# Optimization experiments

Measured on AMD Instinct MI355X. Metric: run time of the kernel, lower is better.

The kernel has to match this reference:

```python
import jax, jax.numpy as jnp
import numpy as np
import math

B, N, D = 8, 4096, 768
H, M, L = 12, 64, 4
HD = D // H  # 64
TEMP = 1.0
EPS = 1e-5


def layer_norm(x, g, b):
    m = jnp.mean(x, axis=-1, keepdims=True)
    v = jnp.mean((x - m) ** 2, axis=-1, keepdims=True)
    return (x - m) * jax.lax.rsqrt(v + EPS) * g + b


def setup_inputs() -> dict:
    key = jax.random.key(0)
    ks = jax.random.split(key, 24)
    s = 0.02
    inp = {
        "latent_tokens": jax.random.normal(ks[0], (B, N, D), jnp.float32),
        "selector": jax.random.normal(ks[1], (M, D), jnp.float32) * s,
        "qc": jax.random.normal(ks[2], (L, M, D), jnp.float32) * s,
        "qw": jax.random.normal(ks[3], (L, H, D, HD), jnp.float32) * s,
        "qb": jnp.zeros((L, H, HD), jnp.float32),
        "kw": jax.random.normal(ks[4], (L, H, D, HD), jnp.float32) * s,
        "kb": jnp.zeros((L, H, HD), jnp.float32),
        "vw": jax.random.normal(ks[5], (L, H, D, HD), jnp.float32) * s,
        "vb": jnp.zeros((L, H, HD), jnp.float32),
        "hw": jax.random.normal(ks[6], (L, H, HD, HD), jnp.float32) * s,
        "hb": jnp.zeros((L, H, HD), jnp.float32),
        "ow": jax.random.normal(ks[7], (L, D, D), jnp.float32) * s,
        "ob": jnp.zeros((L, D), jnp.float32),
        "w1": jax.random.normal(ks[8], (L, D, 4 * D), jnp.float32) * s,
        "b1": jnp.zeros((L, 4 * D), jnp.float32),
        "w2": jax.random.normal(ks[9], (L, 4 * D, D), jnp.float32) * s,
        "b2": jnp.zeros((L, D), jnp.float32),
        "g1": jnp.ones((L, D), jnp.float32),
        "beta1": jnp.zeros((L, D), jnp.float32),
        "g2": jnp.ones((L, D), jnp.float32),
        "beta2": jnp.zeros((L, D), jnp.float32),
    }
    return inp


def reference(latent_tokens, selector, qc, qw, qb, kw, kb, vw, vb, hw, hb,
              ow, ob, w1, b1, w2, b2, g1, beta1, g2, beta2):
    scale = 1.0 / math.sqrt(HD)
    # soft-selection pooling of encoder tokens into M pos queries
    logits = jnp.einsum('bnd,md->bmn', latent_tokens, selector)
    weights = jax.nn.softmax(logits / TEMP, axis=-1)
    x = jnp.einsum('bmn,bnd->bmd', weights, latent_tokens)  # [B,M,D]
    for l in range(L):
        queries = qc[l][None] + x                                    # [B,M,D]
        q = jnp.einsum('bmd,hde->bhme', queries, qw[l]) + qb[l][None, :, None, :]
        k = jnp.einsum('bnd,hde->bhne', latent_tokens, kw[l]) + kb[l][None, :, None, :]
        v = jnp.einsum('bnd,hde->bhne', latent_tokens, vw[l]) + vb[l][None, :, None, :]
        attn = jax.nn.softmax(jnp.einsum('bhme,bhne->bhmn', q, k) * scale, axis=-1)
        o = jnp.einsum('bhmn,bhne->bhme', attn, v)                   # [B,H,M,HD]
        o = jnp.einsum('bhme,hef->bhmf', o, hw[l]) + hb[l][None, :, None, :]
        o = o.transpose(0, 2, 1, 3).reshape(o.shape[0], M, D)        # concat heads
        o = o @ ow[l] + ob[l]
        x1 = layer_norm(o + queries, g1[l], beta1[l])
        mlp = jax.nn.gelu(x1 @ w1[l] + b1[l], approximate=False) @ w2[l] + b2[l]
        x = layer_norm(x1 + mlp, g2[l], beta2[l])
    return x
```

## Files before the change

### kernel.cpp

```cpp
#include <hip/hip_runtime.h>
#include <hip/hip_bf16.h>


using bf16 = __hip_bfloat16;
typedef __attribute__((ext_vector_type(8))) __bf16 bf16x8;
typedef __attribute__((ext_vector_type(4))) float f32x4;
typedef unsigned int u32;
typedef __attribute__((ext_vector_type(4))) u32 u32x4;

#define DEVINL __device__ __forceinline__

DEVINL float bf2f(bf16 v) { return __bfloat162float(v); }
DEVINL bf16 f2bf(float v) { return __float2bfloat16(v); }
DEVINL u32 f2bfu(float f) { bf16 h = __float2bfloat16(f); return *(unsigned short*)&h; }
DEVINL float gelu_f(float x) { return 0.5f * x * (1.0f + erff(x * 0.70710678118654752f)); }

DEVINL void async16(const bf16* g, bf16* l) {
  __builtin_amdgcn_global_load_lds(
      (const __attribute__((address_space(1))) u32*)g,
      (__attribute__((address_space(3))) u32*)l, 16, 0, 0);
}

DEVINL u32 xcd_swizzle(u32 id, u32 nwg) {
  u32 q = nwg >> 3, r = nwg & 7;
  u32 xcd = id & 7, pos = id >> 3;
  return xcd * q + (xcd < r ? xcd : r) + pos;
}

__global__ __launch_bounds__(256) void cvt_f2b(const float* in, bf16* out, long n) {
  const long i = ((long)blockIdx.x * 256 + threadIdx.x) * 8;
  if (i >= n) return;
  float4 a = *(const float4*)(in + i);
  float4 b = *(const float4*)(in + i + 4);
  u32 w[4];
  w[0] = f2bfu(a.x) | (f2bfu(a.y) << 16);
  w[1] = f2bfu(a.z) | (f2bfu(a.w) << 16);
  w[2] = f2bfu(b.x) | (f2bfu(b.y) << 16);
  w[3] = f2bfu(b.z) | (f2bfu(b.w) << 16);
  *(u32x4*)(out + i) = *(u32x4*)w;
}

struct GemmKVP {
  const bf16* A;
  const bf16* Bk;
  const bf16* Bv;
  bf16* Ck;
  bf16* Cv;
  const float* biask;
  const float* biasv;
};

__global__ __launch_bounds__(256, 2) void gemm_kv(GemmKVP p) {
  __shared__ __align__(16) bf16 SH[40960];
  bf16* As = SH;
  bf16* Ks = SH + 16384;
  bf16* Vs = SH + 28672;
  const int tid = threadIdx.x;
  const int wave = tid >> 6, lane = tid & 63;

  u32 id = blockIdx.x + 6u * blockIdx.y;
  id = xcd_swizzle(id, 1536);
  const int bn = id % 6;
  const int bm = id / 6;

  const bf16* Ag = p.A + (long)bm * 128 * 768;
  const bf16* Kg = p.Bk + (long)bn * 128 * 768;
  const bf16* Vg = p.Bv + (long)bn * 128 * 768;

  const int cq = (((tid & 3) ^ ((tid >> 3) & 3))) * 8;
  const long ro = (long)(tid >> 2) * 768 + cq;
  const long r1 = ro + (long)64 * 768;
  const bf16* ga0 = Ag + ro; const bf16* ga1 = Ag + r1;
  const bf16* gk0 = Kg + ro; const bf16* gk1 = Kg + r1;
  const bf16* gv0 = Vg + ro; const bf16* gv1 = Vg + r1;

  const int m_in = lane & 15, q = lane >> 4;
  const int wm = (wave & 1) * 64, wn = (wave >> 1) * 64;
  const int sw3 = (q ^ ((m_in >> 1) & 3)) << 3;
  f32x4 acck[4][4] = {};
  f32x4 accv[4][4] = {};
  const int nk = 24;

  auto stageA = [&](int s, int ko) {
    async16(ga0 + ko, As + s * 4096 + tid * 8);
    async16(ga1 + ko, As + s * 4096 + 2048 + tid * 8);
  };
  auto stageKV = [&](int s, int ko) {
    async16(gk0 + ko, Ks + s * 4096 + tid * 8);
    async16(gk1 + ko, Ks + s * 4096 + 2048 + tid * 8);
    async16(gv0 + ko, Vs + s * 4096 + tid * 8);
    async16(gv1 + ko, Vs + s * 4096 + 2048 + tid * 8);
  };
  stageA(0, 0); stageA(1, 32); stageKV(0, 0); stageA(2, 64); stageKV(1, 32);

  for (int k = 0; k < nk; ++k) {
    if (k < nk - 2)       asm volatile("s_waitcnt vmcnt(6)" ::: "memory");
    else if (k == nk - 2) asm volatile("s_waitcnt vmcnt(4)" ::: "memory");
    else                  asm volatile("s_waitcnt vmcnt(0)" ::: "memory");
    __builtin_amdgcn_s_barrier();
    if (k + 3 < nk) stageA((k + 3) & 3, (k + 3) * 32);
    if (k + 2 < nk) stageKV((k + 2) % 3, (k + 2) * 32);
    const bf16* Ac = As + (k & 3) * 4096;
    const bf16* Kc = Ks + (k % 3) * 4096;
    const bf16* Vc = Vs + (k % 3) * 4096;
    bf16x8 af[4], bfr[4];
#pragma unroll
    for (int i = 0; i < 4; i++)
      af[i] = *(const bf16x8*)(Ac + (wm + i * 16 + m_in) * 32 + sw3);
#pragma unroll
    for (int j = 0; j < 4; j++)
      bfr[j] = *(const bf16x8*)(Kc + (wn + j * 16 + m_in) * 32 + sw3);
#pragma unroll
    for (int i = 0; i < 4; i++)
#pragma unroll
      for (int j = 0; j < 4; j++)
        acck[i][j] = __builtin_amdgcn_mfma_f32_16x16x32_bf16(af[i], bfr[j], acck[i][j], 0, 0, 0);
#pragma unroll
    for (int j = 0; j < 4; j++)
      bfr[j] = *(const bf16x8*)(Vc + (wn + j * 16 + m_in) * 32 + sw3);
#pragma unroll
    for (int i = 0; i < 4; i++)
#pragma unroll
      for (int j = 0; j < 4; j++)
        accv[i][j] = __builtin_amdgcn_mfma_f32_16x16x32_bf16(af[i], bfr[j], accv[i][j], 0, 0, 0);
  }

  const long row0 = (long)bm * 128 + wm + q * 4;
  const long col0 = (long)bn * 128 + wn + m_in;
  const int bb = (bm * 128) >> 12;
  const int nn0 = (bm * 128) & 4095;
#pragma unroll
  for (int i = 0; i < 4; i++)
#pragma unroll
    for (int j = 0; j < 4; j++) {
      long r = row0 + i * 16;
      long c = col0 + j * 16;
      float bk_ = p.biask[c];
#pragma unroll
      for (int t = 0; t < 4; t++)
        p.Ck[(r + t) * 768 + c] = f2bf(acck[i][j][t] + bk_);
    }
  __syncthreads();
  bf16* VT = SH;
#pragma unroll
  for (int i = 0; i < 4; i++) {
    const int nb = wm + q * 4 + i * 16;
    const int sl = nb >> 3;
    const int of = nb & 7;
#pragma unroll
    for (int j = 0; j < 4; j++) {
      const int e = wn + j * 16 + m_in;
      const float bv_ = p.biasv[bn * 128 + e];
      u32 w0 = f2bfu(accv[i][j][0] + bv_) | (f2bfu(accv[i][j][1] + bv_) << 16);
      u32 w1 = f2bfu(accv[i][j][2] + bv_) | (f2bfu(accv[i][j][3] + bv_) << 16);
      uint2 pk; pk.x = w0; pk.y = w1;
      *(uint2*)(VT + e * 128 + ((sl ^ (e & 15)) << 3) + of) = pk;
    }
  }
  __syncthreads();
  bf16* CvB = p.Cv + (long)bb * 3145728;
#pragma unroll
  for (int k2 = 0; k2 < 8; k2++) {
    int g = tid + k2 * 256;
    int e = g >> 4, sc = g & 15;
    u32x4 vv = *(const u32x4*)(VT + e * 128 + ((sc ^ (e & 15)) << 3));
    *(u32x4*)(CvB + (long)(bn * 128 + e) * 4096 + nn0 + sc * 8) = vv;
  }
}

struct GemmSmP {
  const bf16* A; const bf16* B; void* C; const float* bias; const float* res;
  long sA1, sA2, sB1, sB2, sC1, sC2, sBias2;
  int nb2, lda, ldb, ldc, K;
  int bias_mode;
  int out_mode;
  float scale;
};

__global__ __launch_bounds__(256, 4) void gemm_sm(GemmSmP p) {
  __shared__ __align__(16) bf16 As[3][64 * 32];
  __shared__ __align__(16) bf16 Bs[3][64 * 32];
  const int tid = threadIdx.x;
  const int wave = tid >> 6, lane = tid & 63;

  const u32 gx = gridDim.x, gy = gridDim.y;
  u32 id = blockIdx.x + gx * (blockIdx.y + gy * blockIdx.z);
  id = xcd_swizzle(id, gx * gy * gridDim.z);
  const int bn = id % gx;
  const u32 t2 = id / gx;
  const int bm = t2 % gy;
  const int bz = t2 / gy;

  const int z1 = bz / p.nb2, z2 = bz - z1 * p.nb2;
  const bf16* Ag = p.A + p.sA1 * z1 + p.sA2 * z2 + (long)bm * 64 * p.lda;
  const bf16* Bg = p.B + p.sB1 * z1 + p.sB2 * z2 + (long)bn * 64 * p.ldb;

  const int cq = (((tid & 3) ^ ((tid >> 3) & 3))) * 8;
  const bf16* gpa = Ag + ((long)(tid >> 2) * p.lda + cq);
  const bf16* gpb = Bg + ((long)(tid >> 2) * p.ldb + cq);

  const int m_in = lane & 15, q = lane >> 4;
  const int wm = (wave & 1) * 32, wn = (wave >> 1) * 32;
  const int sw3 = (q ^ ((m_in >> 1) & 3)) << 3;
  f32x4 acc[2][2] = {};
  const int nk = p.K >> 5;

  async16(gpa, &As[0][0] + tid * 8);
  async16(gpb, &Bs[0][0] + tid * 8);
  if (nk > 1) {
    async16(gpa + 32, &As[1][0] + tid * 8);
    async16(gpb + 32, &Bs[1][0] + tid * 8);
  }

  int slot = 0;
  for (int k = 0; k < nk; ++k) {
    if (k + 1 < nk) asm volatile("s_waitcnt vmcnt(2)" ::: "memory");
    else            asm volatile("s_waitcnt vmcnt(0)" ::: "memory");
    __builtin_amdgcn_s_barrier();
    if (k + 2 < nk) {
      int ns = slot + 2; if (ns >= 3) ns -= 3;
      const int ko = (k + 2) * 32;
      async16(gpa + ko, &As[ns][0] + tid * 8);
      async16(gpb + ko, &Bs[ns][0] + tid * 8);
    }
    const bf16* Ac = &As[slot][0];
    const bf16* Bc = &Bs[slot][0];
    bf16x8 a0 = *(const bf16x8*)(Ac + (wm + m_in) * 32 + sw3);
    bf16x8 a1 = *(const bf16x8*)(Ac + (wm + 16 + m_in) * 32 + sw3);
    bf16x8 b0 = *(const bf16x8*)(Bc + (wn + m_in) * 32 + sw3);
    bf16x8 b1 = *(const bf16x8*)(Bc + (wn + 16 + m_in) * 32 + sw3);
    acc[0][0] = __builtin_amdgcn_mfma_f32_16x16x32_bf16(a0, b0, acc[0][0], 0, 0, 0);
    acc[0][1] = __builtin_amdgcn_mfma_f32_16x16x32_bf16(a0, b1, acc[0][1], 0, 0, 0);
    acc[1][0] = __builtin_amdgcn_mfma_f32_16x16x32_bf16(a1, b0, acc[1][0], 0, 0, 0);
    acc[1][1] = __builtin_amdgcn_mfma_f32_16x16x32_bf16(a1, b1, acc[1][1], 0, 0, 0);
    slot = (slot + 1 == 3) ? 0 : slot + 1;
  }

  const long row0 = (long)bm * 64 + wm + q * 4;
  const long col0 = (long)bn * 64 + wn + m_in;
  const float* bias = p.bias + p.sBias2 * z2;
#pragma unroll
  for (int i = 0; i < 2; i++)
#pragma unroll
    for (int j = 0; j < 2; j++) {
      long r = row0 + i * 16;
      long cc = col0 + j * 16;
      float badd = (p.bias_mode == 1) ? bias[cc] : 0.f;
#pragma unroll
      for (int t = 0; t < 4; t++) {
        float v = acc[i][j][t] * p.scale + badd;
        long idx = (r + t) * p.ldc + cc;
        if (p.out_mode == 0) {
          float* Cf = (float*)p.C + p.sC1 * z1 + p.sC2 * z2;
          if (p.res) v += p.res[idx];
          Cf[idx] = v;
        } else {
          bf16* Cb = (bf16*)p.C + p.sC1 * z1 + p.sC2 * z2;
          if (p.out_mode == 2) v = gelu_f(v);
          Cb[idx] = f2bf(v);
        }
      }
    }
}

struct AttnP {
  const bf16* Q;
  const bf16* K;
  const bf16* VT;
  float* Opart;
  float* ML;
};

__global__ __launch_bounds__(256, 3) void attn_part(AttnP p) {
  __shared__ __align__(16) bf16 SH[24576];
  bf16* Qs = SH;
  bf16* Ks = SH + 4096;
  bf16* Vs = SH + 12288;
  bf16* Ps = SH + 20480;
  const int tid = threadIdx.x;
  const int wave = tid >> 6, lane = tid & 63;
  const int z = blockIdx.x, c = blockIdx.y;
  const int b = z / 12, h = z - b * 12;
  const int n0 = c * 512;

  const int sl0 = tid, sl1 = tid + 256;
  const int r0 = sl0 >> 3, r1 = sl1 >> 3;
  const int q0 = (sl0 & 7) ^ (r0 & 7), q1 = (sl1 & 7) ^ (r1 & 7);

  const bf16* Qg = p.Q + ((long)b * 64) * 768 + h * 64;
  const bf16* Kg = p.K + ((long)b * 4096 + n0) * 768 + h * 64;
  const bf16* Vg = p.VT + (long)b * 3145728 + (long)(h * 64) * 4096 + n0;

  async16(Qg + (long)r0 * 768 + q0 * 8, Qs + sl0 * 8);
  async16(Qg + (long)r1 * 768 + q1 * 8, Qs + sl1 * 8);
  auto stageK = [&](int s) {
    bf16* d = Ks + (s & 1) * 4096;
    async16(Kg + (long)(s * 64 + r0) * 768 + q0 * 8, d + sl0 * 8);
    async16(Kg + (long)(s * 64 + r1) * 768 + q1 * 8, d + sl1 * 8);
  };
  auto stageV = [&](int s) {
    bf16* d = Vs + (s & 1) * 4096;
    async16(Vg + (long)r0 * 4096 + s * 64 + q0 * 8, d + sl0 * 8);
    async16(Vg + (long)r1 * 4096 + s * 64 + q1 * 8, d + sl1 * 8);
  };
  stageK(0); stageV(0); stageK(1); stageV(1);

  const int m_in = lane & 15, q = lane >> 4;
  const int wm = wave * 16;

  asm volatile("s_waitcnt vmcnt(8)" ::: "memory");
  __builtin_amdgcn_s_barrier();

  bf16x8 qa[2];
  {
    const int ra = wm + m_in;
#pragma unroll
    for (int kk = 0; kk < 2; kk++)
      qa[kk] = *(const bf16x8*)(Qs + ra * 64 + ((((kk * 4 + q) ^ (ra & 7))) << 3));
  }

  f32x4 accO[4] = {};
  float m_run[4] = {-1e30f, -1e30f, -1e30f, -1e30f};
  float l_run[4] = {0.f, 0.f, 0.f, 0.f};

  for (int s = 0; s < 8; ++s) {
    if (s < 7) asm volatile("s_waitcnt vmcnt(4)" ::: "memory");
    else       asm volatile("s_waitcnt vmcnt(0)" ::: "memory");
    __builtin_amdgcn_s_barrier();
    const bf16* Kc = Ks + (s & 1) * 4096;
    const bf16* Vc = Vs + (s & 1) * 4096;
    f32x4 accS[4] = {};
#pragma unroll
    for (int kk = 0; kk < 2; kk++) {
#pragma unroll
      for (int j = 0; j < 4; j++) {
        const int rj = j * 16 + m_in;
        bf16x8 kb = *(const bf16x8*)(Kc + rj * 64 + ((((kk * 4 + q) ^ (rj & 7))) << 3));
        accS[j] = __builtin_amdgcn_mfma_f32_16x16x32_bf16(qa[kk], kb, accS[j], 0, 0, 0);
      }
    }
    float pe[4][4], osc[4];
#pragma unroll
    for (int t = 0; t < 4; t++) {
      float mx = fmaxf(fmaxf(accS[0][t], accS[1][t]), fmaxf(accS[2][t], accS[3][t])) * 0.125f;
      mx = fmaxf(mx, __shfl_xor(mx, 1));
      mx = fmaxf(mx, __shfl_xor(mx, 2));
      mx = fmaxf(mx, __shfl_xor(mx, 4));
      mx = fmaxf(mx, __shfl_xor(mx, 8));
      const float mnew = fmaxf(m_run[t], mx);
      const float so = __expf(m_run[t] - mnew);
      float rs = 0.f;
#pragma unroll
      for (int j = 0; j < 4; j++) {
        float e = __expf(accS[j][t] * 0.125f - mnew);
        pe[j][t] = e; rs += e;
      }
      rs += __shfl_xor(rs, 1); rs += __shfl_xor(rs, 2);
      rs += __shfl_xor(rs, 4); rs += __shfl_xor(rs, 8);
      l_run[t] = l_run[t] * so + rs;
      m_run[t] = mnew;
      osc[t] = so;
    }
#pragma unroll
    for (int ef = 0; ef < 4; ef++)
#pragma unroll
      for (int t = 0; t < 4; t++) accO[ef][t] *= osc[t];
#pragma unroll
    for (int j = 0; j < 4; j++) {
      const int pc = m_in + 16 * j;
#pragma unroll
      for (int t = 0; t < 4; t++) {
        const int pm = wm + q * 4 + t;
        Ps[pm * 64 + (((pc >> 3) ^ (pm & 7)) << 3) + (pc & 7)] = f2bf(pe[j][t]);
      }
    }
    const int ra = wm + m_in;
#pragma unroll
    for (int kk = 0; kk < 2; kk++) {
      bf16x8 pa = *(const bf16x8*)(Ps + ra * 64 + ((((kk * 4 + q) ^ (ra & 7))) << 3));
#pragma unroll
      for (int ef = 0; ef < 4; ef++) {
        const int rv = ef * 16 + m_in;
        bf16x8 vb = *(const bf16x8*)(Vc + rv * 64 + ((((kk * 4 + q) ^ (rv & 7))) << 3));
        accO[ef] = __builtin_amdgcn_mfma_f32_16x16x32_bf16(pa, vb, accO[ef], 0, 0, 0);
      }
    }
    __builtin_amdgcn_s_barrier();
    if (s < 6) { stageK(s + 2); stageV(s + 2); }
  }

  float* Og = p.Opart + ((long)c * 96 + z) * 4096;
#pragma unroll
  for (int ef = 0; ef < 4; ef++)
#pragma unroll
    for (int t = 0; t < 4; t++)
      Og[(wm + q * 4 + t) * 64 + ef * 16 + m_in] = accO[ef][t];
  if (m_in == 0) {
    float* ml = p.ML + ((long)c * 96 + z) * 128;
#pragma unroll
    for (int t = 0; t < 4; t++) {
      ml[wm + q * 4 + t] = m_run[t];
      ml[64 + wm + q * 4 + t] = l_run[t];
    }
  }
}

struct AttnHMP {
  const float* Opart;
  const float* ML;
  const bf16* HWT;
  const float* hb;
  bf16* O2;
};

__global__ __launch_bounds__(256) void attn_hm(AttnHMP p) {
  __shared__ __align__(16) bf16 Os[4096];
  __shared__ __align__(16) bf16 Hs[4096];
  const int tid = threadIdx.x;
  const int z = blockIdx.x;
  const int b = z / 12, h = z - b * 12;

  const int sl0 = tid, sl1 = tid + 256;
  const int r0 = sl0 >> 3, r1 = sl1 >> 3;
  const int q0 = (sl0 & 7) ^ (r0 & 7), q1 = (sl1 & 7) ^ (r1 & 7);
  const bf16* Hg = p.HWT + h * 4096;
  async16(Hg + r0 * 64 + q0 * 8, Hs + sl0 * 8);
  async16(Hg + r1 * 64 + q1 * 8, Hs + sl1 * 8);

  const int m = tid >> 2, e0 = (tid & 3) * 16;
  float mv[8];
  float mx = -1e30f;
#pragma unroll
  for (int c = 0; c < 8; c++) {
    mv[c] = p.ML[((long)c * 96 + z) * 128 + m];
    mx = fmaxf(mx, mv[c]);
  }
  float l = 0.f;
  float o[16] = {};
#pragma unroll
  for (int c = 0; c < 8; c++) {
    const float w = __expf(mv[c] - mx);
    l += w * p.ML[((long)c * 96 + z) * 128 + 64 + m];
    const float* Og = p.Opart + (((long)c * 96 + z) * 64 + m) * 64 + e0;
#pragma unroll
    for (int e = 0; e < 16; e++) o[e] += w * Og[e];
  }
  const float inv = 1.f / l;
#pragma unroll
  for (int half = 0; half < 2; half++) {
    u32 wbuf[4];
#pragma unroll
    for (int j = 0; j < 4; j++)
      wbuf[j] = f2bfu(o[half * 8 + 2 * j] * inv) | (f2bfu(o[half * 8 + 2 * j + 1] * inv) << 16);
    const int sl = (e0 >> 3) + half;
    *(u32x4*)(Os + m * 64 + ((sl ^ (m & 7)) << 3)) = *(u32x4*)wbuf;
  }
  asm volatile("s_waitcnt vmcnt(0)" ::: "memory");
  __syncthreads();

  const int wave = tid >> 6, lane = tid & 63;
  const int m_in = lane & 15, q = lane >> 4;
  const int wm = wave * 16;
  f32x4 acc[4] = {};
#pragma unroll
  for (int kk = 0; kk < 2; kk++) {
    const int ra = wm + m_in;
    bf16x8 a = *(const bf16x8*)(Os + ra * 64 + ((((kk * 4 + q) ^ (ra & 7))) << 3));
#pragma unroll
    for (int j = 0; j < 4; j++) {
      const int rb = j * 16 + m_in;
      bf16x8 bv = *(const bf16x8*)(Hs + rb * 64 + ((((kk * 4 + q) ^ (rb & 7))) << 3));
      acc[j] = __builtin_amdgcn_mfma_f32_16x16x32_bf16(a, bv, acc[j], 0, 0, 0);
    }
  }
  bf16* O2r = p.O2 + ((long)b * 64) * 768 + h * 64;
#pragma unroll
  for (int j = 0; j < 4; j++) {
    const int e2 = j * 16 + m_in;
    const float badd = p.hb[h * 64 + e2];
#pragma unroll
    for (int t = 0; t < 4; t++)
      O2r[(wm + q * 4 + t) * 768 + e2] = f2bf(acc[j][t] + badd);
  }
}

struct TrP { const float* in; bf16* out; bf16* outR; int R, C; long sIn, sOut, sOutR; };

__global__ __launch_bounds__(256) void transpose_f2b(TrP p) {
  __shared__ __align__(16) bf16 tile[64][80];
  const int tid = threadIdx.x;
  const int ct = blockIdx.x, rt = blockIdx.y, z = blockIdx.z;
  const float* in = p.in + p.sIn * z + ((long)rt * 64) * p.C + (long)ct * 64;
  bf16* out = p.out + p.sOut * z + ((long)ct * 64) * p.R + (long)rt * 64;
  bf16* outR = p.outR ? p.outR + p.sOutR * z + ((long)rt * 64) * p.C + (long)ct * 64 : nullptr;
  const int r = tid >> 3, c8 = (tid & 7) * 8;
#pragma unroll
  for (int h = 0; h < 2; h++) {
    int rr = r + h * 32;
    float4 a = *(const float4*)(in + (long)rr * p.C + c8);
    float4 b = *(const float4*)(in + (long)rr * p.C + c8 + 4);
    u32 w[4];
    w[0] = f2bfu(a.x) | (f2bfu(a.y) << 16);
    w[1] = f2bfu(a.z) | (f2bfu(a.w) << 16);
    w[2] = f2bfu(b.x) | (f2bfu(b.y) << 16);
    w[3] = f2bfu(b.z) | (f2bfu(b.w) << 16);
    *(u32x4*)&tile[rr][c8] = *(u32x4*)w;
    if (outR) *(u32x4*)(outR + (long)rr * p.C + c8) = *(u32x4*)w;
  }
  __syncthreads();
  const int co = tid >> 3, r8 = (tid & 7) * 8;
#pragma unroll
  for (int h = 0; h < 2; h++) {
    int cc = co + h * 32;
    __align__(16) bf16 tmp[8];
#pragma unroll
    for (int j = 0; j < 8; j++) tmp[j] = tile[r8 + j][cc];
    *(u32x4*)(out + (long)cc * p.R + r8) = *(const u32x4*)tmp;
  }
}

__global__ __launch_bounds__(256) void softmax_rows(bf16* X) {
  const long row = blockIdx.x;
  u32* x = (u32*)(X + row * 4096);
  const int tid = threadIdx.x;
  const int lane = tid & 63, wave = tid >> 6;
  u32 d[8];
  *(u32x4*)&d[0] = ((const u32x4*)x)[tid * 2];
  *(u32x4*)&d[4] = ((const u32x4*)x)[tid * 2 + 1];
  float v[16];
#pragma unroll
  for (int j = 0; j < 8; j++) {
    v[2 * j] = __uint_as_float(d[j] << 16);
    v[2 * j + 1] = __uint_as_float(d[j] & 0xffff0000u);
  }
  float m = v[0];
#pragma unroll
  for (int i = 1; i < 16; i++) m = fmaxf(m, v[i]);
  for (int off = 32; off; off >>= 1) m = fmaxf(m, __shfl_xor(m, off));
  __shared__ float sm1[4], sm2[4];
  if (lane == 0) sm1[wave] = m;
  __syncthreads();
  m = fmaxf(fmaxf(sm1[0], sm1[1]), fmaxf(sm1[2], sm1[3]));
  float s = 0.f;
#pragma unroll
  for (int i = 0; i < 16; i++) { v[i] = __expf(v[i] - m); s += v[i]; }
  for (int off = 32; off; off >>= 1) s += __shfl_xor(s, off);
  if (lane == 0) sm2[wave] = s;
  __syncthreads();
  s = sm2[0] + sm2[1] + sm2[2] + sm2[3];
  const float inv = 1.f / s;
#pragma unroll
  for (int j = 0; j < 8; j++) {
    u32 lo = f2bfu(v[2 * j] * inv);
    u32 hi = f2bfu(v[2 * j + 1] * inv);
    d[j] = lo | (hi << 16);
  }
  ((u32x4*)x)[tid * 2] = *(u32x4*)&d[0];
  ((u32x4*)x)[tid * 2 + 1] = *(u32x4*)&d[4];
}

__global__ __launch_bounds__(256) void ln_rows(const float* in, const float* g, const float* b,
                                               float* outf, bf16* outb,
                                               const float* qc, float* qf, bf16* qb16) {
  const long row = blockIdx.x;
  const float* x = in + row * 768;
  const int tid = threadIdx.x;
  const int lane = tid & 63, wave = tid >> 6;
  float v0 = x[tid], v1 = x[tid + 256], v2 = x[tid + 512];
  float s = v0 + v1 + v2;
  float s2 = v0 * v0 + v1 * v1 + v2 * v2;
  for (int off = 32; off; off >>= 1) { s += __shfl_xor(s, off); s2 += __shfl_xor(s2, off); }
  __shared__ float sa[4], sb[4];
  if (lane == 0) { sa[wave] = s; sb[wave] = s2; }
  __syncthreads();
  s = sa[0] + sa[1] + sa[2] + sa[3];
  s2 = sb[0] + sb[1] + sb[2] + sb[3];
  const float mean = s * (1.f / 768.f);
  const float var = s2 * (1.f / 768.f) - mean * mean;
  const float rs = rsqrtf(var + 1e-5f);
  float o0 = (v0 - mean) * rs * g[tid] + b[tid];
  float o1 = (v1 - mean) * rs * g[tid + 256] + b[tid + 256];
  float o2 = (v2 - mean) * rs * g[tid + 512] + b[tid + 512];
  if (outf) { float* of = outf + row * 768; of[tid] = o0; of[tid + 256] = o1; of[tid + 512] = o2; }
  if (outb) { bf16* ob = outb + row * 768; ob[tid] = f2bf(o0); ob[tid + 256] = f2bf(o1); ob[tid + 512] = f2bf(o2); }
  if (qc) {
    const float* qr = qc + (row & 63) * 768;
    float u0 = o0 + qr[tid], u1 = o1 + qr[tid + 256], u2 = o2 + qr[tid + 512];
    float* pf = qf + row * 768;
    pf[tid] = u0; pf[tid + 256] = u1; pf[tid + 512] = u2;
    bf16* pb = qb16 + row * 768;
    pb[tid] = f2bf(u0); pb[tid + 256] = f2bf(u1); pb[tid + 512] = f2bf(u2);
  }
}

struct CombLnP {
  const float* in; int nch; const float* bias; const float* res;
  const float* g; const float* b;
  float* outf; bf16* outb;
  const float* qc; float* qf; bf16* qb16;
};

__global__ __launch_bounds__(256) void comb_ln(CombLnP p) {
  const long row = blockIdx.x;
  const long base = row * 768;
  const int tid = threadIdx.x;
  const int lane = tid & 63, wave = tid >> 6;
  float v0 = 0.f, v1 = 0.f, v2 = 0.f;
  for (int c = 0; c < p.nch; c++) {
    const float* x = p.in + (long)c * 393216 + base;
    v0 += x[tid]; v1 += x[tid + 256]; v2 += x[tid + 512];
  }
  v0 += p.bias[tid]; v1 += p.bias[tid + 256]; v2 += p.bias[tid + 512];
  if (p.res) {
    const float* r = p.res + base;
    v0 += r[tid]; v1 += r[tid + 256]; v2 += r[tid + 512];
  }
  float s = v0 + v1 + v2;
  float s2 = v0 * v0 + v1 * v1 + v2 * v2;
  for (int off = 32; off; off >>= 1) { s += __shfl_xor(s, off); s2 += __shfl_xor(s2, off); }
  __shared__ float sa[4], sb[4];
  if (lane == 0) { sa[wave] = s; sb[wave] = s2; }
  __syncthreads();
  s = sa[0] + sa[1] + sa[2] + sa[3];
  s2 = sb[0] + sb[1] + sb[2] + sb[3];
  const float mean = s * (1.f / 768.f);
  const float var = s2 * (1.f / 768.f) - mean * mean;
  const float rs = rsqrtf(var + 1e-5f);
  float o0 = (v0 - mean) * rs * p.g[tid] + p.b[tid];
  float o1 = (v1 - mean) * rs * p.g[tid + 256] + p.b[tid + 256];
  float o2 = (v2 - mean) * rs * p.g[tid + 512] + p.b[tid + 512];
  if (p.outf) { float* of = p.outf + base; of[tid] = o0; of[tid + 256] = o1; of[tid + 512] = o2; }
  if (p.outb) { bf16* ob = p.outb + base; ob[tid] = f2bf(o0); ob[tid + 256] = f2bf(o1); ob[tid + 512] = f2bf(o2); }
  if (p.qc) {
    const float* qr = p.qc + (row & 63) * 768;
    float u0 = o0 + qr[tid], u1 = o1 + qr[tid + 256], u2 = o2 + qr[tid + 512];
    float* pf = p.qf + base;
    pf[tid] = u0; pf[tid + 256] = u1; pf[tid + 512] = u2;
    bf16* pb = p.qb16 + base;
    pb[tid] = f2bf(u0); pb[tid + 256] = f2bf(u1); pb[tid + 512] = f2bf(u2);
  }
}

struct CombP { const float* in; int nch; const float* bias; const float* res;
               float* outf; bf16* outb; const float* qc; float* qf; bf16* qb16; };

__global__ __launch_bounds__(256) void combine(CombP p) {
  const long i = (long)blockIdx.x * 256 + threadIdx.x;
  float s = 0.f;
  for (int c = 0; c < p.nch; c++) s += p.in[(long)c * 393216 + i];
  if (p.bias) s += p.bias[i % 768];
  if (p.res) s += p.res[i];
  if (p.outf) p.outf[i] = s;
  if (p.outb) p.outb[i] = f2bf(s);
  if (p.qc) {
    float v = s + p.qc[i % 49152];
    p.qf[i] = v;
    p.qb16[i] = f2bf(v);
  }
}

extern "C" void kernel_launch(void* const* d_in, const int* in_sizes, int n_in,
                              void* d_out, int out_size, void* d_ws, size_t ws_size,
                              hipStream_t stream) {
  (void)in_sizes; (void)n_in; (void)out_size; (void)ws_size;
  const float* tokens   = (const float*)d_in[0];
  const float* selector = (const float*)d_in[1];
  const float* qc  = (const float*)d_in[2];
  const float* qw  = (const float*)d_in[3];
  const float* qb  = (const float*)d_in[4];
  const float* kw  = (const float*)d_in[5];
  const float* kb  = (const float*)d_in[6];
  const float* vw  = (const float*)d_in[7];
  const float* vb  = (const float*)d_in[8];
  const float* hw  = (const float*)d_in[9];
  const float* hb  = (const float*)d_in[10];
  const float* ow  = (const float*)d_in[11];
  const float* ob  = (const float*)d_in[12];
  const float* w1  = (const float*)d_in[13];
  const float* b1  = (const float*)d_in[14];
  const float* w2  = (const float*)d_in[15];
  const float* b2  = (const float*)d_in[16];
  const float* g1  = (const float*)d_in[17];
  const float* be1 = (const float*)d_in[18];
  const float* g2  = (const float*)d_in[19];
  const float* be2 = (const float*)d_in[20];
  float* out = (float*)d_out;

  char* ws = (char*)d_ws;
  size_t off = 0;
  auto alloc = [&](size_t bytes) { char* pp = ws + off; off += (bytes + 255) & ~(size_t)255; return pp; };
  bf16* TOKT  = (bf16*)alloc(50331648);
  bf16* TOKB  = (bf16*)alloc(50331648);
  bf16* KBUF  = (bf16*)alloc(50331648);
  bf16* VTB   = (bf16*)alloc(50331648);
  bf16* PLOG  = (bf16*)alloc(4194304);
  bf16* SELB  = (bf16*)alloc(98304);
  bf16* QWT   = (bf16*)alloc(4718592);
  bf16* KWT   = (bf16*)alloc(4718592);
  bf16* VWT   = (bf16*)alloc(4718592);
  bf16* HWT   = (bf16*)alloc(393216);
  bf16* OWT   = (bf16*)alloc(4718592);
  bf16* W1T   = (bf16*)alloc(18874368);
  bf16* W2T   = (bf16*)alloc(18874368);
  bf16* QBUF  = (bf16*)alloc(786432);
  bf16* O2BUF = (bf16*)alloc(786432);
  float* QF   = (float*)alloc(1572864);
  bf16* QB16  = (bf16*)alloc(786432);
  float* X1F  = (float*)alloc(1572864);
  bf16* X1B   = (bf16*)alloc(786432);
  bf16* H1    = (bf16*)alloc(3145728);
  float* OPART = (float*)alloc(12582912);
  float* MLB  = (float*)alloc(393216);

  auto tr = [&](const float* in, bf16* o, bf16* oR, int R, int C, long s, long sR, int slabs) {
    TrP t{in, o, oR, R, C, s, s, sR};
    transpose_f2b<<<dim3(C / 64, R / 64, slabs), 256, 0, stream>>>(t);
  };
  tr(tokens, TOKT, TOKB, 4096, 768, 3145728, 3145728, 8);
  cvt_f2b<<<24, 256, 0, stream>>>(selector, SELB, 49152);
  tr(qw, QWT, nullptr, 768, 64, 49152, 0, 48);
  tr(kw, KWT, nullptr, 768, 64, 49152, 0, 48);
  tr(vw, VWT, nullptr, 768, 64, 49152, 0, 48);
  tr(hw, HWT, nullptr, 64, 64, 4096, 0, 48);
  tr(ow, OWT, nullptr, 768, 768, 589824, 0, 4);
  tr(w1, W1T, nullptr, 768, 3072, 2359296, 0, 4);
  tr(w2, W2T, nullptr, 3072, 768, 2359296, 0, 4);

  {
    GemmSmP p{}; p.A = SELB; p.B = TOKB; p.C = PLOG;
    p.sB1 = 3145728; p.sC1 = 262144; p.nb2 = 1;
    p.lda = 768; p.ldb = 768; p.ldc = 4096; p.K = 768;
    p.bias_mode = 0; p.out_mode = 1; p.scale = 1.0f;
    gemm_sm<<<dim3(64, 1, 8), 256, 0, stream>>>(p);
  }
  softmax_rows<<<512, 256, 0, stream>>>(PLOG);
  {
    GemmSmP p{}; p.A = PLOG; p.B = TOKT; p.C = OPART;
    p.sA1 = 512; p.sA2 = 262144; p.sB1 = 512; p.sB2 = 3145728;
    p.sC1 = 393216; p.sC2 = 49152; p.nb2 = 8;
    p.lda = 4096; p.ldb = 4096; p.ldc = 768; p.K = 512;
    p.bias_mode = 0; p.out_mode = 0; p.scale = 1.0f;
    gemm_sm<<<dim3(12, 1, 64), 256, 0, stream>>>(p);
  }
  {
    CombP c{}; c.in = OPART; c.nch = 8; c.qc = qc; c.qf = QF; c.qb16 = QB16;
    combine<<<1536, 256, 0, stream>>>(c);
  }

  for (int l = 0; l < 4; l++) {
    {
      GemmSmP p{}; p.A = QB16; p.B = QWT + l * 589824; p.C = QBUF; p.bias = qb + l * 768;
      p.nb2 = 1; p.lda = 768; p.ldb = 768; p.ldc = 768; p.K = 768;
      p.bias_mode = 1; p.out_mode = 1; p.scale = 1.0f;
      gemm_sm<<<dim3(12, 8, 1), 256, 0, stream>>>(p);
    }
    {
      GemmKVP p{TOKB, KWT + l * 589824, VWT + l * 589824, KBUF, VTB,
                kb + l * 768, vb + l * 768};
      gemm_kv<<<dim3(6, 256, 1), 256, 0, stream>>>(p);
    }
    {
      AttnP p{QBUF, KBUF, VTB, OPART, MLB};
      attn_part<<<dim3(96, 8, 1), 256, 0, stream>>>(p);
    }
    {
      AttnHMP p{OPART, MLB, HWT + l * 49152, hb + l * 768, O2BUF};
      attn_hm<<<96, 256, 0, stream>>>(p);
    }
    {
      GemmSmP p{}; p.A = O2BUF; p.B = OWT + l * 589824; p.C = OPART;
      p.sA1 = 192; p.sB1 = 192; p.sC1 = 393216; p.nb2 = 1;
      p.lda = 768; p.ldb = 768; p.ldc = 768; p.K = 192;
      p.bias_mode = 0; p.out_mode = 0; p.scale = 1.0f;
      gemm_sm<<<dim3(12, 8, 4), 256, 0, stream>>>(p);
    }
    {
      CombLnP c{}; c.in = OPART; c.nch = 4; c.bias = ob + l * 768; c.res = QF;
      c.g = g1 + l * 768; c.b = be1 + l * 768; c.outf = X1F; c.outb = X1B;
      comb_ln<<<512, 256, 0, stream>>>(c);
    }
    {
      GemmSmP p{}; p.A = X1B; p.B = W1T + l * 2359296; p.C = H1; p.bias = b1 + l * 3072;
      p.nb2 = 1; p.lda = 768; p.ldb = 768; p.ldc = 3072; p.K = 768;
      p.bias_mode = 1; p.out_mode = 2; p.scale = 1.0f;
      gemm_sm<<<dim3(48, 8, 1), 256, 0, stream>>>(p);
    }
    {
      GemmSmP p{}; p.A = H1; p.B = W2T + l * 2359296; p.C = OPART;
      p.sA1 = 384; p.sB1 = 384; p.sC1 = 393216; p.nb2 = 1;
      p.lda = 3072; p.ldb = 3072; p.ldc = 768; p.K = 384;
      p.bias_mode = 0; p.out_mode = 0; p.scale = 1.0f;
      gemm_sm<<<dim3(12, 8, 8), 256, 0, stream>>>(p);
    }
    {
      CombLnP c{}; c.in = OPART; c.nch = 8; c.bias = b2 + l * 768; c.res = X1F;
      c.g = g2 + l * 768; c.b = be2 + l * 768;
      c.outf = (l == 3) ? out : nullptr;
      c.qc = (l < 3) ? (qc + (l + 1) * 49152) : nullptr;
      c.qf = QF; c.qb16 = QB16;
      comb_ln<<<512, 256, 0, stream>>>(c);
    }
  }
}
```

Baseline: 1.075 ms.

## Split K and V accumulation across separate wave groups in fused KV GEMM

The fused K/V projection GEMM goes from 256 to 512 threads per block. Half the waves now accumulate K and half accumulate V, so each wave keeps one accumulator set instead of two. That lowers register pressure and allows higher occupancy (launch bounds 512,4). The pipeline is simplified to a uniform 3-stage buffer for A, K and V, which cuts shared memory, though the shared A tile is now read by twice as many waves. An unused layernorm kernel is also removed.

```diff
diff --git a/kernel.cpp b/kernel.cpp
--- a/kernel.cpp
+++ b/kernel.cpp
@@ -50,11 +50,11 @@
   const float* biasv;
 };
 
-__global__ __launch_bounds__(256, 2) void gemm_kv(GemmKVP p) {
-  __shared__ __align__(16) bf16 SH[40960];
+__global__ __launch_bounds__(512, 4) void gemm_kv(GemmKVP p) {
+  __shared__ __align__(16) bf16 SH[36864];
   bf16* As = SH;
-  bf16* Ks = SH + 16384;
-  bf16* Vs = SH + 28672;
+  bf16* Ks = SH + 12288;
+  bf16* Vs = SH + 24576;
   const int tid = threadIdx.x;
   const int wave = tid >> 6, lane = tid & 63;
 
@@ -69,99 +69,88 @@
 
   const int cq = (((tid & 3) ^ ((tid >> 3) & 3))) * 8;
   const long ro = (long)(tid >> 2) * 768 + cq;
-  const long r1 = ro + (long)64 * 768;
-  const bf16* ga0 = Ag + ro; const bf16* ga1 = Ag + r1;
-  const bf16* gk0 = Kg + ro; const bf16* gk1 = Kg + r1;
-  const bf16* gv0 = Vg + ro; const bf16* gv1 = Vg + r1;
+  const bf16* ga = Ag + ro;
+  const bf16* gk = Kg + ro;
+  const bf16* gv = Vg + ro;
 
   const int m_in = lane & 15, q = lane >> 4;
-  const int wm = (wave & 1) * 64, wn = (wave >> 1) * 64;
+  const int wstream = wave >> 2;
+  const int wq = wave & 3;
+  const int wm = (wq & 1) * 64, wn = (wq >> 1) * 64;
   const int sw3 = (q ^ ((m_in >> 1) & 3)) << 3;
-  f32x4 acck[4][4] = {};
-  f32x4 accv[4][4] = {};
+  f32x4 acc[4][4] = {};
   const int nk = 24;
 
-  auto stageA = [&](int s, int ko) {
-    async16(ga0 + ko, As + s * 4096 + tid * 8);
-    async16(ga1 + ko, As + s * 4096 + 2048 + tid * 8);
+  auto stage = [&](int s, int ko) {
+    async16(ga + ko, As + s * 4096 + tid * 8);
+    async16(gk + ko, Ks + s * 4096 + tid * 8);
+    async16(gv + ko, Vs + s * 4096 + tid * 8);
   };
-  auto stageKV = [&](int s, int ko) {
-    async16(gk0 + ko, Ks + s * 4096 + tid * 8);
-    async16(gk1 + ko, Ks + s * 4096 + 2048 + tid * 8);
-    async16(gv0 + ko, Vs + s * 4096 + tid * 8);
-    async16(gv1 + ko, Vs + s * 4096 + 2048 + tid * 8);
-  };
-  stageA(0, 0); stageA(1, 32); stageKV(0, 0); stageA(2, 64); stageKV(1, 32);
+  stage(0, 0);
+  stage(1, 32);
 
   for (int k = 0; k < nk; ++k) {
-    if (k < nk - 2)       asm volatile("s_waitcnt vmcnt(6)" ::: "memory");
-    else if (k == nk - 2) asm volatile("s_waitcnt vmcnt(4)" ::: "memory");
-    else                  asm volatile("s_waitcnt vmcnt(0)" ::: "memory");
+    if (k + 1 < nk) asm volatile("s_waitcnt vmcnt(3)" ::: "memory");
+    else            asm volatile("s_waitcnt vmcnt(0)" ::: "memory");
     __builtin_amdgcn_s_barrier();
-    if (k + 3 < nk) stageA((k + 3) & 3, (k + 3) * 32);
-    if (k + 2 < nk) stageKV((k + 2) % 3, (k + 2) * 32);
-    const bf16* Ac = As + (k & 3) * 4096;
-    const bf16* Kc = Ks + (k % 3) * 4096;
-    const bf16* Vc = Vs + (k % 3) * 4096;
+    if (k + 2 < nk) stage((k + 2) % 3, (k + 2) * 32);
+    const bf16* Ac = As + (k % 3) * 4096;
+    const bf16* Bc = (wstream == 0 ? Ks : Vs) + (k % 3) * 4096;
     bf16x8 af[4], bfr[4];
 #pragma unroll
     for (int i = 0; i < 4; i++)
       af[i] = *(const bf16x8*)(Ac + (wm + i * 16 + m_in) * 32 + sw3);
 #pragma unroll
     for (int j = 0; j < 4; j++)
-      bfr[j] = *(const bf16x8*)(Kc + (wn + j * 16 + m_in) * 32 + sw3);
+      bfr[j] = *(const bf16x8*)(Bc + (wn + j * 16 + m_in) * 32 + sw3);
 #pragma unroll
     for (int i = 0; i < 4; i++)
 #pragma unroll
       for (int j = 0; j < 4; j++)
-        acck[i][j] = __builtin_amdgcn_mfma_f32_16x16x32_bf16(af[i], bfr[j], acck[i][j], 0, 0, 0);
-#pragma unroll
-    for (int j = 0; j < 4; j++)
-      bfr[j] = *(const bf16x8*)(Vc + (wn + j * 16 + m_in) * 32 + sw3);
-#pragma unroll
-    for (int i = 0; i < 4; i++)
-#pragma unroll
-      for (int j = 0; j < 4; j++)
-        accv[i][j] = __builtin_amdgcn_mfma_f32_16x16x32_bf16(af[i], bfr[j], accv[i][j], 0, 0, 0);
-  }
-
-  const long row0 = (long)bm * 128 + wm + q * 4;
-  const long col0 = (long)bn * 128 + wn + m_in;
+        acc[i][j] = __builtin_amdgcn_mfma_f32_16x16x32_bf16(af[i], bfr[j], acc[i][j], 0, 0, 0);
+  }
+
   const int bb = (bm * 128) >> 12;
   const int nn0 = (bm * 128) & 4095;
-#pragma unroll
-  for (int i = 0; i < 4; i++)
-#pragma unroll
-    for (int j = 0; j < 4; j++) {
-      long r = row0 + i * 16;
-      long c = col0 + j * 16;
-      float bk_ = p.biask[c];
-#pragma unroll
-      for (int t = 0; t < 4; t++)
-        p.Ck[(r + t) * 768 + c] = f2bf(acck[i][j][t] + bk_);
-    }
   __syncthreads();
-  bf16* VT = SH;
-#pragma unroll
-  for (int i = 0; i < 4; i++) {
-    const int nb = wm + q * 4 + i * 16;
-    const int sl = nb >> 3;
-    const int of = nb & 7;
-#pragma unroll
-    for (int j = 0; j < 4; j++) {
-      const int e = wn + j * 16 + m_in;
-      const float bv_ = p.biasv[bn * 128 + e];
-      u32 w0 = f2bfu(accv[i][j][0] + bv_) | (f2bfu(accv[i][j][1] + bv_) << 16);
-      u32 w1 = f2bfu(accv[i][j][2] + bv_) | (f2bfu(accv[i][j][3] + bv_) << 16);
-      uint2 pk; pk.x = w0; pk.y = w1;
-      *(uint2*)(VT + e * 128 + ((sl ^ (e & 15)) << 3) + of) = pk;
+  if (wstream == 0) {
+    const long row0 = (long)bm * 128 + wm + q * 4;
+    const long col0 = (long)bn * 128 + wn + m_in;
+#pragma unroll
+    for (int i = 0; i < 4; i++)
+#pragma unroll
+      for (int j = 0; j < 4; j++) {
+        long r = row0 + i * 16;
+        long c = col0 + j * 16;
+        float bk_ = p.biask[c];
+#pragma unroll
+        for (int t = 0; t < 4; t++)
+          p.Ck[(r + t) * 768 + c] = f2bf(acc[i][j][t] + bk_);
+      }
+  } else {
+    bf16* VT = SH;
+#pragma unroll
+    for (int i = 0; i < 4; i++) {
+      const int nb = wm + q * 4 + i * 16;
+      const int sl = nb >> 3;
+      const int of = nb & 7;
+#pragma unroll
+      for (int j = 0; j < 4; j++) {
+        const int e = wn + j * 16 + m_in;
+        const float bv_ = p.biasv[bn * 128 + e];
+        u32 w0 = f2bfu(acc[i][j][0] + bv_) | (f2bfu(acc[i][j][1] + bv_) << 16);
+        u32 w1 = f2bfu(acc[i][j][2] + bv_) | (f2bfu(acc[i][j][3] + bv_) << 16);
+        uint2 pk; pk.x = w0; pk.y = w1;
+        *(uint2*)(VT + e * 128 + ((sl ^ (e & 15)) << 3) + of) = pk;
+      }
     }
   }
   __syncthreads();
   bf16* CvB = p.Cv + (long)bb * 3145728;
-#pragma unroll
-  for (int k2 = 0; k2 < 8; k2++) {
-    int g = tid + k2 * 256;
+  const bf16* VT = SH;
+#pragma unroll
+  for (int k2 = 0; k2 < 4; k2++) {
+    int g = tid + k2 * 512;
     int e = g >> 4, sc = g & 15;
     u32x4 vv = *(const u32x4*)(VT + e * 128 + ((sc ^ (e & 15)) << 3));
     *(u32x4*)(CvB + (long)(bn * 128 + e) * 4096 + nn0 + sc * 8) = vv;
@@ -557,40 +546,6 @@
   }
   ((u32x4*)x)[tid * 2] = *(u32x4*)&d[0];
   ((u32x4*)x)[tid * 2 + 1] = *(u32x4*)&d[4];
-}
-
-__global__ __launch_bounds__(256) void ln_rows(const float* in, const float* g, const float* b,
-                                               float* outf, bf16* outb,
-                                               const float* qc, float* qf, bf16* qb16) {
-  const long row = blockIdx.x;
-  const float* x = in + row * 768;
-  const int tid = threadIdx.x;
-  const int lane = tid & 63, wave = tid >> 6;
-  float v0 = x[tid], v1 = x[tid + 256], v2 = x[tid + 512];
-  float s = v0 + v1 + v2;
-  float s2 = v0 * v0 + v1 * v1 + v2 * v2;
-  for (int off = 32; off; off >>= 1) { s += __shfl_xor(s, off); s2 += __shfl_xor(s2, off); }
-  __shared__ float sa[4], sb[4];
-  if (lane == 0) { sa[wave] = s; sb[wave] = s2; }
-  __syncthreads();
-  s = sa[0] + sa[1] + sa[2] + sa[3];
-  s2 = sb[0] + sb[1] + sb[2] + sb[3];
-  const float mean = s * (1.f / 768.f);
-  const float var = s2 * (1.f / 768.f) - mean * mean;
-  const float rs = rsqrtf(var + 1e-5f);
-  float o0 = (v0 - mean) * rs * g[tid] + b[tid];
-  float o1 = (v1 - mean) * rs * g[tid + 256] + b[tid + 256];
-  float o2 = (v2 - mean) * rs * g[tid + 512] + b[tid + 512];
-  if (outf) { float* of = outf + row * 768; of[tid] = o0; of[tid + 256] = o1; of[tid + 512] = o2; }
-  if (outb) { bf16* ob = outb + row * 768; ob[tid] = f2bf(o0); ob[tid + 256] = f2bf(o1); ob[tid + 512] = f2bf(o2); }
-  if (qc) {
-    const float* qr = qc + (row & 63) * 768;
-    float u0 = o0 + qr[tid], u1 = o1 + qr[tid + 256], u2 = o2 + qr[tid + 512];
-    float* pf = qf + row * 768;
-    pf[tid] = u0; pf[tid + 256] = u1; pf[tid + 512] = u2;
-    bf16* pb = qb16 + row * 768;
-    pb[tid] = f2bf(u0); pb[tid + 256] = f2bf(u1); pb[tid + 512] = f2bf(u2);
-  }
 }
 
 struct CombLnP {
@@ -757,7 +712,7 @@
     {
       GemmKVP p{TOKB, KWT + l * 589824, VWT + l * 589824, KBUF, VTB,
                 kb + l * 768, vb + l * 768};
-      gemm_kv<<<dim3(6, 256, 1), 256, 0, stream>>>(p);
+      gemm_kv<<<dim3(6, 256, 1), 512, 0, stream>>>(p);
     }
     {
       AttnP p{QBUF, KBUF, VTB, OPART, MLB};
```

Result: no change. 1.057 ms (-1.6%).
